# Optimization experiments

Hardware: AMD Instinct MI355X
Metric: run time of the kernel (lower is better)

## Reference

```python
import jax, jax.numpy as jnp
import numpy as np

B, T, D, H = 2, 2048, 1024, 16
HD = D // H  # head_dim = 64

def setup_inputs() -> dict:
    key = jax.random.key(0)
    ks = jax.random.split(key, 6)
    s = 1.0 / np.sqrt(D)
    return {
        "x": jax.random.normal(ks[0], (B, T, D), jnp.float32),
        "Wq": jax.random.normal(ks[1], (D, D), jnp.float32) * s,
        "Wk": jax.random.normal(ks[2], (D, D), jnp.float32) * s,
        "Wv": jax.random.normal(ks[3], (D, D), jnp.float32) * s,
        "Wo": jax.random.normal(ks[4], (D, D), jnp.float32) * s,
        "bo": jnp.zeros((D,), jnp.float32),
    }

def reference(x, Wq, Wk, Wv, Wo, bo):
    b, n, _ = x.shape
    # projections -> [b, h, n, hd]
    def split_heads(t):
        return t.reshape(b, n, H, HD).transpose(0, 2, 1, 3)
    q = split_heads(x @ Wq)
    k = split_heads(x @ Wk)
    v = split_heads(x @ Wv)
    scale = HD ** 0.5
    scores = jnp.einsum('bhqd,bhkd->bhqk', q, k) / scale
    causal = jnp.tril(jnp.ones((n, n), bool))  # True = keep
    scores = jnp.where(causal, scores, -jnp.inf)
    attn = jax.nn.softmax(scores, axis=-1)
    ctx = jnp.einsum('bhqk,bhkd->bhqd', attn, v)
    ctx = ctx.transpose(0, 2, 1, 3).reshape(b, n, D)
    return ctx @ Wo + bo
```

## Files before the change

kernel.cpp:

```cpp
#include <hip/hip_runtime.h>
#include <stdint.h>

typedef unsigned short u16;
typedef unsigned int   u32;
typedef __attribute__((ext_vector_type(8))) __bf16 bf8;
typedef __attribute__((ext_vector_type(4))) float  f4;

#define NEG_INF (-__builtin_inff())

#define BB 2
#define TT 2048
#define DD 1024
#define HH 16
#define HD 64
#define BT (BB*TT)

#define SBAR() __builtin_amdgcn_s_barrier()
#define VMCNT4() asm volatile("s_waitcnt vmcnt(4)" ::: "memory")
#define VMCNT0() asm volatile("s_waitcnt vmcnt(0)" ::: "memory")
#define LGKMCNT0() asm volatile("s_waitcnt lgkmcnt(0)" ::: "memory")

__device__ __forceinline__ u16 f2bf(float f) {
  u32 u = __builtin_bit_cast(u32, f);
  u += 0x7FFFu + ((u >> 16) & 1u);
  return (u16)(u >> 16);
}

__device__ __forceinline__ float exp2fast(float x) {
  float r; asm("v_exp_f32 %0, %1" : "=v"(r) : "v"(x)); return r;
}

__device__ __forceinline__ void g2l16(const void* g, void* l) {
  __builtin_amdgcn_global_load_lds((const __attribute__((address_space(1))) u32*)g,
                                   (__attribute__((address_space(3))) u32*)l, 16, 0, 0);
}

__global__ void k_cast_x(const float* __restrict__ x, uint4* __restrict__ xb) {
  int i = blockIdx.x * 256 + threadIdx.x;
  const float4* xf = (const float4*)x;
  float4 a = xf[2*i], b = xf[2*i+1];
  uint4 o;
  o.x = (u32)f2bf(a.x) | ((u32)f2bf(a.y) << 16);
  o.y = (u32)f2bf(a.z) | ((u32)f2bf(a.w) << 16);
  o.z = (u32)f2bf(b.x) | ((u32)f2bf(b.y) << 16);
  o.w = (u32)f2bf(b.z) | ((u32)f2bf(b.w) << 16);
  xb[i] = o;
}

__global__ void k_twcast(const float* __restrict__ w0, const float* __restrict__ w1,
                         const float* __restrict__ w2, const float* __restrict__ w3,
                         u16* __restrict__ o0, u16* __restrict__ o1,
                         u16* __restrict__ o2, u16* __restrict__ o3) {
  const float* W; u16* O;
  switch (blockIdx.z) {
    case 0: W = w0; O = o0; break;
    case 1: W = w1; O = o1; break;
    case 2: W = w2; O = o2; break;
    default: W = w3; O = o3; break;
  }
  __shared__ __align__(16) u16 tile[64][80];
  int tid = threadIdx.x;
  int k0 = blockIdx.y * 64, n0 = blockIdx.x * 64;
#pragma unroll
  for (int it = 0; it < 4; ++it) {
    int c = it*256 + tid; int kr = c >> 4, ns = c & 15;
    float4 v = *(const float4*)(W + (size_t)(k0+kr)*DD + n0 + ns*4);
    u16* p = &tile[kr][ns*4];
    p[0] = f2bf(v.x); p[1] = f2bf(v.y); p[2] = f2bf(v.z); p[3] = f2bf(v.w);
  }
  __syncthreads();
#pragma unroll
  for (int it = 0; it < 2; ++it) {
    int c = it*256 + tid; int nr = c >> 3, ks = c & 7;
    u32 ww[4];
#pragma unroll
    for (int e = 0; e < 4; ++e) {
      u16 lo = tile[ks*8 + 2*e][nr], hi = tile[ks*8 + 2*e + 1][nr];
      ww[e] = (u32)lo | ((u32)hi << 16);
    }
    uint4 o; o.x = ww[0]; o.y = ww[1]; o.z = ww[2]; o.w = ww[3];
    *(uint4*)(O + (size_t)(n0+nr)*DD + k0 + ks*8) = o;
  }
}

__global__ __launch_bounds__(256, 2) void k_qkv(const u16* __restrict__ xb,
    const u16* __restrict__ wqt, const u16* __restrict__ wkt, const u16* __restrict__ wvt,
    u16* __restrict__ qo, u16* __restrict__ ko, u16* __restrict__ vo) {
  __shared__ uint4 smem4[1024];
  char* smem = (char*)smem4;
  int tid = threadIdx.x, w = tid >> 6, l = tid & 63;
  int bid = blockIdx.y * 24 + blockIdx.x;
  int wg = (bid & 7) * 96 + (bid >> 3);
  int nb = wg % 24, mb = wg / 24;
  const u16* Bt = (nb < 8) ? wqt : (nb < 16 ? wkt : wvt);
  int nbl = nb & 7;
  int wm = w >> 1, wn = w & 1;
  f4 z = {0.f, 0.f, 0.f, 0.f};
  f4 acc[4][4];
#pragma unroll
  for (int i = 0; i < 4; ++i)
#pragma unroll
    for (int j = 0; j < 4; ++j) acc[i][j] = z;

  for (int kt = 0; kt < 32; ++kt) {
    int kk = kt * 32;
    __syncthreads();
#pragma unroll
    for (int i = 0; i < 2; ++i) {
      int c = i*256 + tid; int row = c >> 2, u = c & 3, s = u ^ ((row >> 1) & 3);
      g2l16(xb + (size_t)(mb*128 + row)*DD + kk + s*8, smem + (i*256 + w*64)*16);
    }
#pragma unroll
    for (int i = 0; i < 2; ++i) {
      int c = i*256 + tid; int row = c >> 2, u = c & 3, s = u ^ ((row >> 1) & 3);
      g2l16(Bt + (size_t)(nbl*128 + row)*DD + kk + s*8, smem + 8192 + (i*256 + w*64)*16);
    }
    __syncthreads();
    bf8 af[4], bfr[4];
#pragma unroll
    for (int mf = 0; mf < 4; ++mf) {
      int row = wm*64 + mf*16 + (l & 15);
      int s = (l >> 4) ^ ((row >> 1) & 3);
      af[mf] = *(const bf8*)(smem + row*64 + s*16);
    }
#pragma unroll
    for (int nf = 0; nf < 4; ++nf) {
      int row = wn*64 + nf*16 + (l & 15);
      int s = (l >> 4) ^ ((row >> 1) & 3);
      bfr[nf] = *(const bf8*)(smem + 8192 + row*64 + s*16);
    }
#pragma unroll
    for (int mf = 0; mf < 4; ++mf)
#pragma unroll
      for (int nf = 0; nf < 4; ++nf)
        acc[mf][nf] = __builtin_amdgcn_mfma_f32_16x16x32_bf16(af[mf], bfr[nf], acc[mf][nf], 0, 0, 0);
  }
  if (nb < 16) {
    u16* Out = (nb < 8) ? qo : ko;
    float qs = (nb < 8) ? 0.18033688011112042f : 1.0f;
#pragma unroll
    for (int mf = 0; mf < 4; ++mf) {
      int m0 = mb*128 + wm*64 + mf*16 + (l >> 4)*4;
      int b = m0 >> 11;
#pragma unroll
      for (int nf = 0; nf < 4; ++nf) {
        int nn = nbl*128 + wn*64 + nf*16 + (l & 15);
        int h = nn >> 6, d = nn & 63;
#pragma unroll
        for (int r = 0; r < 4; ++r) {
          int t = (m0 + r) & 2047;
          Out[(size_t)((b*HH + h)*TT + t)*HD + d] = f2bf(acc[mf][nf][r] * qs);
        }
      }
    }
  } else {
#pragma unroll
    for (int mf = 0; mf < 4; ++mf) {
      int m0 = mb*128 + wm*64 + mf*16 + (l >> 4)*4;
      int b = m0 >> 11, t0 = m0 & 2047;
#pragma unroll
      for (int nf = 0; nf < 4; ++nf) {
        int nn = nbl*128 + wn*64 + nf*16 + (l & 15);
        int h = nn >> 6, d = nn & 63;
        uint2 o;
        o.x = (u32)f2bf(acc[mf][nf][0]) | ((u32)f2bf(acc[mf][nf][1]) << 16);
        o.y = (u32)f2bf(acc[mf][nf][2]) | ((u32)f2bf(acc[mf][nf][3]) << 16);
        *(uint2*)(vo + (size_t)((b*HH + h)*HD + d)*TT + t0) = o;
      }
    }
  }
}

__global__ __launch_bounds__(256, 2) void k_attn(const u16* __restrict__ q,
    const u16* __restrict__ kk, const u16* __restrict__ vt, u16* __restrict__ ctx) {
  __shared__ __align__(16) char smem[50176];
  int tid = threadIdx.x, w = tid >> 6, l = tid & 63;
  int qi = l & 15, g = l >> 4;
  int fid = blockIdx.x;
  int xcd = fid & 7, j = fid >> 3;
  int bh  = xcd * 4 + (j & 3);
  int ip  = j >> 2;
  u32* Pw = (u32*)(smem + 32768) + w * 1088;
  int b = bh >> 4, h = bh & 15;
  int rot2 = 2 * (qi & 7);

  auto stageK = [&](int t) {
#pragma unroll
    for (int i = 0; i < 4; ++i) {
      int c = i*256 + tid; int row = c >> 3, u = c & 7;
      g2l16(kk + (size_t)(bh*TT + t*128 + row)*HD + (u ^ (row & 7))*8,
            smem + (i*256 + w*64)*16);
    }
  };
  auto stageV = [&](int t) {
#pragma unroll
    for (int i = 0; i < 4; ++i) {
      int c = i*256 + tid; int row = c >> 4, u = c & 15;
      g2l16(vt + (size_t)(bh*HD + row)*TT + t*128 + (u ^ (row & 15))*8,
            smem + 16384 + (i*256 + w*64)*16);
    }
  };

  for (int ps = 0; ps < 2; ++ps) {
    int q0 = (ps ? (31 - ip) : ip) * 64;
    int qw = q0 + w * 16;
    int qrow = qw + qi;
    const u16* qbase = q + (size_t)(bh*TT + qrow)*HD + g*8;
    bf8 qf0 = *(const bf8*)(qbase);
    bf8 qf1 = *(const bf8*)(qbase + 32);
    float mreg = NEG_INF, lreg = 0.f;
    f4 z = {0.f, 0.f, 0.f, 0.f};
    f4 acc[4]; acc[0] = z; acc[1] = z; acc[2] = z; acc[3] = z;
    int nt = (q0 >> 7) + 1;
    stageK(0); stageV(0);
    for (int t = 0; t < nt; ++t) {
      bool last = (t == nt - 1);
      VMCNT4();
      SBAR();
      __builtin_amdgcn_s_setprio(1);
      f4 sv[8];
#pragma unroll
      for (int jf = 0; jf < 8; ++jf) {
        f4 s = z;
        int row = jf*16 + qi;
        int s0 = g ^ (row & 7);
        int s1 = (g + 4) ^ (row & 7);
        bf8 b0 = *(const bf8*)(smem + row*128 + s0*16);
        bf8 b1 = *(const bf8*)(smem + row*128 + s1*16);
        s = __builtin_amdgcn_mfma_f32_16x16x32_bf16(b0, qf0, s, 0, 0, 0);
        s = __builtin_amdgcn_mfma_f32_16x16x32_bf16(b1, qf1, s, 0, 0, 0);
        sv[jf] = s;
      }
      __builtin_amdgcn_s_setprio(0);
      LGKMCNT0();
      SBAR();
      if (!last) stageK(t + 1);
      if (t*128 + 127 > qw) {
        int cbase = qrow - t*128 - 4*g;
#pragma unroll
        for (int jf = 0; jf < 8; ++jf)
#pragma unroll
          for (int r = 0; r < 4; ++r)
            if (jf*16 + r > cbase) sv[jf][r] = NEG_INF;
      }
      float mx = NEG_INF;
#pragma unroll
      for (int jf = 0; jf < 8; ++jf)
        mx = fmaxf(mx, fmaxf(fmaxf(sv[jf][0], sv[jf][1]), fmaxf(sv[jf][2], sv[jf][3])));
      mx = fmaxf(mx, __shfl_xor(mx, 16, 64));
      mx = fmaxf(mx, __shfl_xor(mx, 32, 64));
      float mnew = fmaxf(mreg, mx);
      float alpha = exp2fast(mreg - mnew);
      mreg = mnew;
      float rs = 0.f;
#pragma unroll
      for (int jf = 0; jf < 8; ++jf) {
        float p0 = exp2fast(sv[jf][0] - mreg);
        float p1 = exp2fast(sv[jf][1] - mreg);
        float p2 = exp2fast(sv[jf][2] - mreg);
        float p3 = exp2fast(sv[jf][3] - mreg);
        rs += (p0 + p1) + (p2 + p3);
        uint2 pv;
        pv.x = (u32)f2bf(p0) | ((u32)f2bf(p1) << 16);
        pv.y = (u32)f2bf(p2) | ((u32)f2bf(p3) << 16);
        int blk = 2*jf + (g >> 1);
        *(uint2*)(&Pw[qi*68 + 4*((blk + rot2) & 15) + 2*(g & 1)]) = pv;
      }
      rs += __shfl_xor(rs, 16, 64);
      rs += __shfl_xor(rs, 32, 64);
      lreg = lreg * alpha + rs;
#pragma unroll
      for (int df = 0; df < 4; ++df) {
        f4 a = acc[df];
        a[0] *= alpha; a[1] *= alpha; a[2] *= alpha; a[3] *= alpha;
        acc[df] = a;
      }
      if (!last) { VMCNT4(); } else { VMCNT0(); }
      SBAR();
      __builtin_amdgcn_s_setprio(1);
#pragma unroll
      for (int ks = 0; ks < 4; ++ks) {
        bf8 pf = *(const bf8*)(&Pw[qi*68 + 4*(((4*ks + g) + rot2) & 15)]);
#pragma unroll
        for (int df = 0; df < 4; ++df) {
          int row = df*16 + qi;
          int sl = (ks*4 + g) ^ (row & 15);
          bf8 vf = *(const bf8*)(smem + 16384 + row*256 + sl*16);
          acc[df] = __builtin_amdgcn_mfma_f32_16x16x32_bf16(vf, pf, acc[df], 0, 0, 0);
        }
      }
      __builtin_amdgcn_s_setprio(0);
      LGKMCNT0();
      SBAR();
      if (!last) stageV(t + 1);
    }
    float inv = 1.0f / lreg;
    u16* dst = ctx + (size_t)(b*TT + qrow)*DD + h*HD;
#pragma unroll
    for (int df = 0; df < 4; ++df) {
      uint2 o;
      o.x = (u32)f2bf(acc[df][0] * inv) | ((u32)f2bf(acc[df][1] * inv) << 16);
      o.y = (u32)f2bf(acc[df][2] * inv) | ((u32)f2bf(acc[df][3] * inv) << 16);
      *(uint2*)(dst + df*16 + 4*g) = o;
    }
  }
}

__global__ __launch_bounds__(256, 2) void k_out(const u16* __restrict__ ctx,
    const u16* __restrict__ wot, const float* __restrict__ bo, float* __restrict__ out) {
  __shared__ uint4 smem4[1024];
  char* smem = (char*)smem4;
  int tid = threadIdx.x, w = tid >> 6, l = tid & 63;
  int bid = blockIdx.y * 8 + blockIdx.x;
  int wg = (bid & 7) * 32 + (bid >> 3);
  int nb = wg % 8, mb = wg / 8;
  int wm = w >> 1, wn = w & 1;
  f4 z = {0.f, 0.f, 0.f, 0.f};
  f4 acc[4][4];
#pragma unroll
  for (int i = 0; i < 4; ++i)
#pragma unroll
    for (int j = 0; j < 4; ++j) acc[i][j] = z;

  for (int kt = 0; kt < 32; ++kt) {
    int kkk = kt * 32;
    __syncthreads();
#pragma unroll
    for (int i = 0; i < 2; ++i) {
      int c = i*256 + tid; int row = c >> 2, u = c & 3, s = u ^ ((row >> 1) & 3);
      g2l16(ctx + (size_t)(mb*128 + row)*DD + kkk + s*8, smem + (i*256 + w*64)*16);
    }
#pragma unroll
    for (int i = 0; i < 2; ++i) {
      int c = i*256 + tid; int row = c >> 2, u = c & 3, s = u ^ ((row >> 1) & 3);
      g2l16(wot + (size_t)(nb*128 + row)*DD + kkk + s*8, smem + 8192 + (i*256 + w*64)*16);
    }
    __syncthreads();
    bf8 af[4], bfr[4];
#pragma unroll
    for (int mf = 0; mf < 4; ++mf) {
      int row = wm*64 + mf*16 + (l & 15);
      int s = (l >> 4) ^ ((row >> 1) & 3);
      af[mf] = *(const bf8*)(smem + row*64 + s*16);
    }
#pragma unroll
    for (int nf = 0; nf < 4; ++nf) {
      int row = wn*64 + nf*16 + (l & 15);
      int s = (l >> 4) ^ ((row >> 1) & 3);
      bfr[nf] = *(const bf8*)(smem + 8192 + row*64 + s*16);
    }
#pragma unroll
    for (int mf = 0; mf < 4; ++mf)
#pragma unroll
      for (int nf = 0; nf < 4; ++nf)
        acc[mf][nf] = __builtin_amdgcn_mfma_f32_16x16x32_bf16(af[mf], bfr[nf], acc[mf][nf], 0, 0, 0);
  }
#pragma unroll
  for (int nf = 0; nf < 4; ++nf) {
    int n = nb*128 + wn*64 + nf*16 + (l & 15);
    float bias = bo[n];
#pragma unroll
    for (int mf = 0; mf < 4; ++mf) {
      int m0 = mb*128 + wm*64 + mf*16 + (l >> 4)*4;
#pragma unroll
      for (int r = 0; r < 4; ++r)
        out[(size_t)(m0 + r)*DD + n] = acc[mf][nf][r] + bias;
    }
  }
}

extern "C" void kernel_launch(void* const* d_in, const int* in_sizes, int n_in,
                              void* d_out, int out_size, void* d_ws, size_t ws_size,
                              hipStream_t stream) {
  const float* x  = (const float*)d_in[0];
  const float* Wq = (const float*)d_in[1];
  const float* Wk = (const float*)d_in[2];
  const float* Wv = (const float*)d_in[3];
  const float* Wo = (const float*)d_in[4];
  const float* bo = (const float*)d_in[5];
  float* out = (float*)d_out;
  char* ws = (char*)d_ws;

  u16* xb  = (u16*)(ws);
  u16* wqt = (u16*)(ws + 8388608);
  u16* wkt = (u16*)(ws + 10485760);
  u16* wvt = (u16*)(ws + 12582912);
  u16* wot = (u16*)(ws + 14680064);
  u16* qb_ = (u16*)(ws + 16777216);
  u16* kb_ = (u16*)(ws + 25165824);
  u16* vtb = (u16*)(ws + 41943040);
  u16* cxb = (u16*)(ws + 50331648);

  k_cast_x<<<dim3(2048), dim3(256), 0, stream>>>(x, (uint4*)xb);
  k_twcast<<<dim3(16, 16, 4), dim3(256), 0, stream>>>(Wq, Wk, Wv, Wo, wqt, wkt, wvt, wot);
  k_qkv<<<dim3(24, 32), dim3(256), 0, stream>>>(xb, wqt, wkt, wvt, qb_, kb_, vtb);
  k_attn<<<dim3(512), dim3(256), 0, stream>>>(qb_, kb_, vtb, cxb);
  k_out<<<dim3(8, 32), dim3(256), 0, stream>>>(cxb, wot, bo, out);
}
```

Measured before the change: 182.5 us.

## Double-buffer LDS in projection GEMMs and shrink output tile to 128x64

```diff
diff --git a/kernel.cpp b/kernel.cpp
--- a/kernel.cpp
+++ b/kernel.cpp
@@ -86,8 +86,7 @@
 __global__ __launch_bounds__(256, 2) void k_qkv(const u16* __restrict__ xb,
     const u16* __restrict__ wqt, const u16* __restrict__ wkt, const u16* __restrict__ wvt,
     u16* __restrict__ qo, u16* __restrict__ ko, u16* __restrict__ vo) {
-  __shared__ uint4 smem4[1024];
-  char* smem = (char*)smem4;
+  __shared__ __align__(16) char smem[32768];
   int tid = threadIdx.x, w = tid >> 6, l = tid & 63;
   int bid = blockIdx.y * 24 + blockIdx.x;
   int wg = (bid & 7) * 96 + (bid >> 3);
@@ -102,38 +101,50 @@
 #pragma unroll
     for (int j = 0; j < 4; ++j) acc[i][j] = z;
 
-  for (int kt = 0; kt < 32; ++kt) {
+  auto stage = [&](int buf, int kt) {
     int kk = kt * 32;
-    __syncthreads();
+    char* dst = smem + buf * 16384;
 #pragma unroll
     for (int i = 0; i < 2; ++i) {
       int c = i*256 + tid; int row = c >> 2, u = c & 3, s = u ^ ((row >> 1) & 3);
-      g2l16(xb + (size_t)(mb*128 + row)*DD + kk + s*8, smem + (i*256 + w*64)*16);
+      g2l16(xb + (size_t)(mb*128 + row)*DD + kk + s*8, dst + (i*256 + w*64)*16);
     }
 #pragma unroll
     for (int i = 0; i < 2; ++i) {
       int c = i*256 + tid; int row = c >> 2, u = c & 3, s = u ^ ((row >> 1) & 3);
-      g2l16(Bt + (size_t)(nbl*128 + row)*DD + kk + s*8, smem + 8192 + (i*256 + w*64)*16);
-    }
-    __syncthreads();
+      g2l16(Bt + (size_t)(nbl*128 + row)*DD + kk + s*8, dst + 8192 + (i*256 + w*64)*16);
+    }
+  };
+
+  stage(0, 0);
+  VMCNT0(); SBAR();
+#pragma unroll 2
+  for (int kt = 0; kt < 32; ++kt) {
+    int cur = kt & 1;
+    if (kt < 31) stage(cur ^ 1, kt + 1);
+    char* buf = smem + cur * 16384;
     bf8 af[4], bfr[4];
 #pragma unroll
     for (int mf = 0; mf < 4; ++mf) {
       int row = wm*64 + mf*16 + (l & 15);
       int s = (l >> 4) ^ ((row >> 1) & 3);
-      af[mf] = *(const bf8*)(smem + row*64 + s*16);
+      af[mf] = *(const bf8*)(buf + row*64 + s*16);
     }
 #pragma unroll
     for (int nf = 0; nf < 4; ++nf) {
       int row = wn*64 + nf*16 + (l & 15);
       int s = (l >> 4) ^ ((row >> 1) & 3);
-      bfr[nf] = *(const bf8*)(smem + 8192 + row*64 + s*16);
-    }
+      bfr[nf] = *(const bf8*)(buf + 8192 + row*64 + s*16);
+    }
+    __builtin_amdgcn_s_setprio(1);
 #pragma unroll
     for (int mf = 0; mf < 4; ++mf)
 #pragma unroll
       for (int nf = 0; nf < 4; ++nf)
         acc[mf][nf] = __builtin_amdgcn_mfma_f32_16x16x32_bf16(af[mf], bfr[nf], acc[mf][nf], 0, 0, 0);
+    __builtin_amdgcn_s_setprio(0);
+    LGKMCNT0();
+    VMCNT0(); SBAR();
   }
   if (nb < 16) {
     u16* Out = (nb < 8) ? qo : ko;
@@ -308,56 +319,64 @@
 
 __global__ __launch_bounds__(256, 2) void k_out(const u16* __restrict__ ctx,
     const u16* __restrict__ wot, const float* __restrict__ bo, float* __restrict__ out) {
-  __shared__ uint4 smem4[1024];
-  char* smem = (char*)smem4;
+  __shared__ __align__(16) char smem[24576];
   int tid = threadIdx.x, w = tid >> 6, l = tid & 63;
-  int bid = blockIdx.y * 8 + blockIdx.x;
-  int wg = (bid & 7) * 32 + (bid >> 3);
-  int nb = wg % 8, mb = wg / 8;
+  int bid = blockIdx.x;
+  int wg = (bid & 7) * 64 + (bid >> 3);
+  int nb = wg % 16, mb = wg / 16;
   int wm = w >> 1, wn = w & 1;
   f4 z = {0.f, 0.f, 0.f, 0.f};
-  f4 acc[4][4];
-#pragma unroll
-  for (int i = 0; i < 4; ++i)
-#pragma unroll
-    for (int j = 0; j < 4; ++j) acc[i][j] = z;
-
-  for (int kt = 0; kt < 32; ++kt) {
-    int kkk = kt * 32;
-    __syncthreads();
+  f4 acc[4][2];
+#pragma unroll
+  for (int i = 0; i < 4; ++i) { acc[i][0] = z; acc[i][1] = z; }
+
+  auto stage = [&](int buf, int kt) {
+    int kk = kt * 32;
+    char* dst = smem + buf * 12288;
 #pragma unroll
     for (int i = 0; i < 2; ++i) {
       int c = i*256 + tid; int row = c >> 2, u = c & 3, s = u ^ ((row >> 1) & 3);
-      g2l16(ctx + (size_t)(mb*128 + row)*DD + kkk + s*8, smem + (i*256 + w*64)*16);
-    }
-#pragma unroll
-    for (int i = 0; i < 2; ++i) {
-      int c = i*256 + tid; int row = c >> 2, u = c & 3, s = u ^ ((row >> 1) & 3);
-      g2l16(wot + (size_t)(nb*128 + row)*DD + kkk + s*8, smem + 8192 + (i*256 + w*64)*16);
-    }
-    __syncthreads();
-    bf8 af[4], bfr[4];
+      g2l16(ctx + (size_t)(mb*128 + row)*DD + kk + s*8, dst + (i*256 + w*64)*16);
+    }
+    {
+      int row = tid >> 2, u = tid & 3, s = u ^ ((row >> 1) & 3);
+      g2l16(wot + (size_t)(nb*64 + row)*DD + kk + s*8, dst + 8192 + (w*64)*16);
+    }
+  };
+
+  stage(0, 0);
+  VMCNT0(); SBAR();
+#pragma unroll 2
+  for (int kt = 0; kt < 32; ++kt) {
+    int cur = kt & 1;
+    if (kt < 31) stage(cur ^ 1, kt + 1);
+    char* buf = smem + cur * 12288;
+    bf8 af[4], bfr[2];
 #pragma unroll
     for (int mf = 0; mf < 4; ++mf) {
       int row = wm*64 + mf*16 + (l & 15);
       int s = (l >> 4) ^ ((row >> 1) & 3);
-      af[mf] = *(const bf8*)(smem + row*64 + s*16);
-    }
-#pragma unroll
-    for (int nf = 0; nf < 4; ++nf) {
-      int row = wn*64 + nf*16 + (l & 15);
+      af[mf] = *(const bf8*)(buf + row*64 + s*16);
+    }
+#pragma unroll
+    for (int nf = 0; nf < 2; ++nf) {
+      int row = wn*32 + nf*16 + (l & 15);
       int s = (l >> 4) ^ ((row >> 1) & 3);
-      bfr[nf] = *(const bf8*)(smem + 8192 + row*64 + s*16);
-    }
+      bfr[nf] = *(const bf8*)(buf + 8192 + row*64 + s*16);
+    }
+    __builtin_amdgcn_s_setprio(1);
 #pragma unroll
     for (int mf = 0; mf < 4; ++mf)
 #pragma unroll
-      for (int nf = 0; nf < 4; ++nf)
+      for (int nf = 0; nf < 2; ++nf)
         acc[mf][nf] = __builtin_amdgcn_mfma_f32_16x16x32_bf16(af[mf], bfr[nf], acc[mf][nf], 0, 0, 0);
-  }
-#pragma unroll
-  for (int nf = 0; nf < 4; ++nf) {
-    int n = nb*128 + wn*64 + nf*16 + (l & 15);
+    __builtin_amdgcn_s_setprio(0);
+    LGKMCNT0();
+    VMCNT0(); SBAR();
+  }
+#pragma unroll
+  for (int nf = 0; nf < 2; ++nf) {
+    int n = nb*64 + wn*32 + nf*16 + (l & 15);
     float bias = bo[n];
 #pragma unroll
     for (int mf = 0; mf < 4; ++mf) {
@@ -395,5 +414,5 @@
   k_twcast<<<dim3(16, 16, 4), dim3(256), 0, stream>>>(Wq, Wk, Wv, Wo, wqt, wkt, wvt, wot);
   k_qkv<<<dim3(24, 32), dim3(256), 0, stream>>>(xb, wqt, wkt, wvt, qb_, kb_, vtb);
   k_attn<<<dim3(512), dim3(256), 0, stream>>>(qb_, kb_, vtb, cxb);
-  k_out<<<dim3(8, 32), dim3(256), 0, stream>>>(cxb, wot, bo, out);
-}
+  k_out<<<dim3(512), dim3(256), 0, stream>>>(cxb, wot, bo, out);
+}
```

New measurement: 174.7 us. -4.3%, faster.
